# Kernel optimization log

Hardware: AMD Instinct MI355X
Metric: run time of the kernel (lower is better)

Reference implementation:

```python
import jax, jax.numpy as jnp
import numpy as np

DIM_HEAD = 32  # from init_kwargs; scale = dim_head**-0.5 per the Triton kernel


def setup_inputs() -> dict:
    key = jax.random.key(0)
    k1, k2 = jax.random.split(key)
    B, N, dim = 16, 8192, 128
    D = 4 * DIM_HEAD  # heads * dim_head
    x = jax.random.normal(k1, (B, N, dim), dtype=jnp.float32)
    # ParameterList of 16 stages, each Parameter is randn(2, dim, D) * 0.02
    qk_weights = jax.random.normal(k2, (16, 2, dim, D), dtype=jnp.float32) * 0.02
    return {"x": x, "qk_weights": qk_weights}


def reference(x, qk_weights):
    """FFT-inspired butterfly attention.

    At stage s (stride = 2**s), positions are grouped into blocks of 2*stride;
    the first `stride` elements of each block are 'a', the next `stride` are
    their butterfly partners 'b' (b = a + stride). Q/K are projected from the
    ORIGINAL x with per-stage weights; v is the running value buffer (init x).
    For each pair, a 2-way softmax over [qa.ka, qa.kb] mixes (va, vb).
    """
    B, N, dim = x.shape
    logN = int(round(np.log2(N)))
    D = qk_weights.shape[-1]
    scale = DIM_HEAD ** -0.5

    v = x
    for s in range(logN):
        stride = 1 << s
        Wq = qk_weights[s, 0]  # (dim, D)
        Wk = qk_weights[s, 1]
        q = jnp.einsum('bnd,de->bne', x, Wq) * scale  # (B,N,D)
        k = jnp.einsum('bnd,de->bne', x, Wk)
        G = N // (2 * stride)
        qr = q.reshape(B, G, 2, stride, D)
        kr = k.reshape(B, G, 2, stride, D)
        vr = v.reshape(B, G, 2, stride, dim)
        qa = qr[:, :, 0]
        ka, kb = kr[:, :, 0], kr[:, :, 1]
        va, vb = vr[:, :, 0], vr[:, :, 1]
        s_aa = jnp.sum(qa * ka, axis=-1)  # (B,G,stride)
        s_ab = jnp.sum(qa * kb, axis=-1)
        attn = jax.nn.softmax(jnp.stack([s_aa, s_ab], axis=-1), axis=-1)
        w0 = attn[..., 0:1]
        w1 = attn[..., 1:2]
        out_a = w0 * va + w1 * vb
        out_b = w1 * va + w0 * vb
        v = jnp.stack([out_a, out_b], axis=2).reshape(B, N, dim)
    return v
```

## Files before the change

kernel.cpp:

```cpp
#include <hip/hip_runtime.h>
#include <hip/hip_bf16.h>


typedef __bf16 bf16x8 __attribute__((ext_vector_type(8)));
typedef float  f32x4  __attribute__((ext_vector_type(4)));

#define XSTR 136
#define XB_BYTES  (128 * XSTR * 2)
#define PREP_LDS  (2 * XB_BYTES)
#define LDS_W2    XB_BYTES

#define XW 128
#define LDS_W4    (128 * XW * 2)

#define LDS_MIX   (128 * 128 * 4)

#define WS_DWT_OFF (512 * 1024)
#define DWT4_BYTES (13 * 1024 * 4 * 64 * 4)
#define WS_NEED4   (WS_DWT_OFF + DWT4_BYTES)

__device__ __forceinline__ float ubits(unsigned int u) {
    union { unsigned int u; float f; } v; v.u = u; return v.f;
}
__device__ __forceinline__ unsigned short f2bf(float f) {
    union { float f; unsigned int u; } v; v.f = f;
    unsigned int u = v.u;
    return (unsigned short)((u + 0x7fffu + ((u >> 16) & 1u)) >> 16);
}
__device__ __forceinline__ int swzr(int r) { return ((r >> 1) ^ (r >> 2)) & 15; }

#define DPP_MOV_F(x, ctrl) \
    __int_as_float(__builtin_amdgcn_update_dpp(0, __float_as_int(x), (ctrl), 0xF, 0xF, true))

__device__ __forceinline__ float xlane_u(float x, int u, int lane) {
    if (u == 0) return DPP_MOV_F(x, 0xB1);
    if (u == 1) return DPP_MOV_F(x, 0x4E);
    if (u == 2) return __int_as_float(__builtin_amdgcn_ds_swizzle(__float_as_int(x), 0x101F));
    if (u == 3) return __int_as_float(__builtin_amdgcn_ds_swizzle(__float_as_int(x), 0x201F));
    if (u == 4) return __int_as_float(__builtin_amdgcn_ds_swizzle(__float_as_int(x), 0x401F));
    return __int_as_float(__builtin_amdgcn_ds_bpermute((lane ^ 32) << 2, __float_as_int(x)));
}

__global__ __launch_bounds__(512)
void prep_kernel(const float* __restrict__ qkw, unsigned short* __restrict__ PT) {
    extern __shared__ char smem[];
    unsigned short* wkb = (unsigned short*)smem;
    unsigned short* wqb = (unsigned short*)(smem + XB_BYTES);
    const int s = blockIdx.x;
    const float* Wq = qkw + (size_t)s * 32768;
    const float* Wk = Wq + 16384;
    const int tid = threadIdx.x;
    const int rl = tid >> 5, c4 = tid & 31;
#pragma unroll
    for (int j = 0; j < 8; ++j) {
        int r = j * 16 + rl;
        float4 vq = ((const float4*)Wq)[r * 32 + c4];
        float4 vk = ((const float4*)Wk)[r * 32 + c4];
        ushort4 uq; uq.x = f2bf(vq.x); uq.y = f2bf(vq.y); uq.z = f2bf(vq.z); uq.w = f2bf(vq.w);
        ushort4 uk; uk.x = f2bf(vk.x); uk.y = f2bf(vk.y); uk.z = f2bf(vk.z); uk.w = f2bf(vk.w);
        *(ushort4*)(wqb + r * XSTR + c4 * 4) = uq;
        *(ushort4*)(wkb + r * XSTR + c4 * 4) = uk;
    }
    __syncthreads();
    const int lane = tid & 63, w = tid >> 6;
    const int lane15 = lane & 15, quad = lane >> 4;
    f32x4 acc[8] = {};
#pragma unroll
    for (int kk = 0; kk < 4; ++kk) {
        bf16x8 a = *(const bf16x8*)(wkb + (w * 16 + lane15) * XSTR + kk * 32 + quad * 8);
#pragma unroll
        for (int ct = 0; ct < 8; ++ct) {
            bf16x8 b = *(const bf16x8*)(wqb + (ct * 16 + lane15) * XSTR + kk * 32 + quad * 8);
            acc[ct] = __builtin_amdgcn_mfma_f32_16x16x32_bf16(a, b, acc[ct], 0, 0, 0);
        }
    }
    unsigned short* dst = PT + s * 16384;
#pragma unroll
    for (int ct = 0; ct < 8; ++ct) {
        const int kkf = ct >> 1;
        const int qf  = (ct & 1) * 2 + (lane15 >> 3);
        const int e   = lane15 & 7;
#pragma unroll
        for (int r = 0; r < 4; ++r) {
            int fi = (w * 4 + kkf) * 64 + qf * 16 + quad * 4 + r;
            dst[fi * 8 + e] = f2bf(acc[ct][r] * 0.17677669529663687f);
        }
    }
}

__device__ __forceinline__ void stage_xb(unsigned short* xb, const float* xsrc,
                                         int tid, int base, int h_off, int rstride) {
    const int rl = tid >> 5, c4 = tid & 31;
#pragma unroll
    for (int j = 0; j < 8; ++j) {
        int i  = j * 16 + rl;
        int gp = base + (i >> 6) * h_off + (i & 63) * rstride;
        float4 val = ((const float4*)xsrc)[gp * 32 + c4];
        ushort4 us; us.x = f2bf(val.x); us.y = f2bf(val.y);
        us.z = f2bf(val.z); us.w = f2bf(val.w);
        *(ushort4*)(xb + i * XSTR + c4 * 4) = us;
    }
}

__device__ __forceinline__ void stage_xb_swz(unsigned short* xb, const float* xsrc,
                                             int tid, int base, int h_off, int rstride) {
    const int rl = tid >> 5, c4 = tid & 31;
#pragma unroll
    for (int j = 0; j < 8; ++j) {
        int i  = j * 16 + rl;
        int gp = base + (i >> 6) * h_off + (i & 63) * rstride;
        float4 val = ((const float4*)xsrc)[gp * 32 + c4];
        ushort4 us; us.x = f2bf(val.x); us.y = f2bf(val.y);
        us.z = f2bf(val.z); us.w = f2bf(val.w);
        int slot = c4 >> 1, half = c4 & 1;
        *(ushort4*)(xb + i * XW + (((slot ^ swzr(i)) << 3) + half * 4)) = us;
    }
}

template<int NS>
__global__ __launch_bounds__(512, 4)
void weights4_kernel(const float* __restrict__ xsrc,
                     const unsigned short* __restrict__ PT,
                     float* __restrict__ dwt,
                     int s0, int base_mul, int h_off, int rstride)
{
    extern __shared__ char smem[];
    unsigned short* xb = (unsigned short*)smem;

    const int tid  = threadIdx.x;
    const int b    = blockIdx.x >> 6;
    const int sub  = blockIdx.x & 63;
    const int base = b * 8192 + sub * base_mul;

    stage_xb_swz(xb, xsrc, tid, base, h_off, rstride);

    const int lane = tid & 63, w = tid >> 6;
    const int lane15 = lane & 15, quad = lane >> 4;
    const int dh = w >> 1;
    const int ph = w & 1;

    __syncthreads();

#pragma unroll
    for (int u = 0; u < NS; ++u) {
        const int t   = 1 << u;
        const int tm1 = t - 1;

        const uint4* Pf = (const uint4*)PT + (size_t)(s0 + u) * 2048;
        uint4 af[2][4];
#pragma unroll
        for (int mt = 0; mt < 2; ++mt)
#pragma unroll
            for (int kk = 0; kk < 4; ++kk)
                af[mt][kk] = Pf[((dh * 2 + mt) * 4 + kk) * 64 + lane];

        f32x4 acc[2][2] = {};
#pragma unroll
        for (int pg = 0; pg < 2; ++pg) {
            const int p  = (ph * 2 + pg) * 16 + lane15;
            const int ar = ((p & ~tm1) << 1) | (p & tm1);
            const int swa = swzr(ar);
            const unsigned short* brow = xb + ar * XW;
#pragma unroll
            for (int kk = 0; kk < 4; ++kk) {
                bf16x8 bfrag = *(const bf16x8*)(brow + (((kk * 4 + quad) ^ swa) << 3));
#pragma unroll
                for (int mt = 0; mt < 2; ++mt) {
                    union { uint4 u; bf16x8 b; } av; av.u = af[mt][kk];
                    acc[mt][pg] = __builtin_amdgcn_mfma_f32_16x16x32_bf16(av.b, bfrag, acc[mt][pg], 0, 0, 0);
                }
            }
        }

        float sm[2];
#pragma unroll
        for (int pg = 0; pg < 2; ++pg) {
            const int p  = (ph * 2 + pg) * 16 + lane15;
            const int ar = ((p & ~tm1) << 1) | (p & tm1);
            const int br = ar + t;
            const int swa = swzr(ar), swb = swzr(br);
            float s = 0.f;
#pragma unroll
            for (int mt = 0; mt < 2; ++mt) {
                const int slot = dh * 4 + mt * 2 + (quad >> 1);
                uint2 ua = *(const uint2*)(xb + ar * XW + (((slot ^ swa) << 3) + (quad & 1) * 4));
                uint2 ub = *(const uint2*)(xb + br * XW + (((slot ^ swb) << 3) + (quad & 1) * 4));
                float a0 = ubits(ua.x << 16), a1 = ubits(ua.x & 0xffff0000u);
                float a2 = ubits(ua.y << 16), a3 = ubits(ua.y & 0xffff0000u);
                float b0 = ubits(ub.x << 16), b1 = ubits(ub.x & 0xffff0000u);
                float b2 = ubits(ub.y << 16), b3 = ubits(ub.y & 0xffff0000u);
                s += acc[mt][pg][0] * (a0 - b0) + acc[mt][pg][1] * (a1 - b1)
                   + acc[mt][pg][2] * (a2 - b2) + acc[mt][pg][3] * (a3 - b3);
            }
            s += xlane_u(s, 4, lane);
            s += xlane_u(s, 5, lane);
            sm[pg] = s;
        }
        float v = (lane & 16) ? sm[1] : sm[0];
        if (lane < 32)
            dwt[(((size_t)(s0 + u) * 1024 + blockIdx.x) * 4 + dh) * 64 + ph * 32 + (lane & 31)] = v;
    }
}

template<int NS>
__global__ __launch_bounds__(512, 4)
void weights2_kernel(const float* __restrict__ xsrc,
                     const unsigned short* __restrict__ PT,
                     float* __restrict__ dwt,
                     int s0, int base_mul, int h_off, int rstride)
{
    extern __shared__ char smem[];
    unsigned short* xb = (unsigned short*)smem;

    const int tid  = threadIdx.x;
    const int b    = blockIdx.x >> 6;
    const int sub  = blockIdx.x & 63;
    const int base = b * 8192 + sub * base_mul;

    stage_xb(xb, xsrc, tid, base, h_off, rstride);

    const int lane = tid & 63, w = tid >> 6;
    const int lane15 = lane & 15, quad = lane >> 4;
    const int nt = w & 3;
    const int mh = w >> 2;
    const int p  = nt * 16 + lane15;

    __syncthreads();

#pragma unroll
    for (int u = 0; u < NS; ++u) {
        const int t   = 1 << u;
        const int tm1 = t - 1;
        const int ar  = ((p & ~tm1) << 1) | (p & tm1);

        float sm = 0.f;
        {
            const uint4* Pf = (const uint4*)PT + (size_t)(s0 + u) * 2048;
            const unsigned short* brow = xb + ar * XSTR + quad * 8;
            f32x4 acc[4] = {};
#pragma unroll
            for (int kk = 0; kk < 4; ++kk) {
                bf16x8 bfrag = *(const bf16x8*)(brow + kk * 32);
#pragma unroll
                for (int mt = 0; mt < 4; ++mt) {
                    union { uint4 u; bf16x8 b; } av;
                    av.u = Pf[((mh * 4 + mt) * 4 + kk) * 64 + lane];
                    acc[mt] = __builtin_amdgcn_mfma_f32_16x16x32_bf16(av.b, bfrag, acc[mt], 0, 0, 0);
                }
            }
            const unsigned short* da = xb + ar * XSTR + mh * 64 + quad * 4;
            const unsigned short* db = da + t * XSTR;
#pragma unroll
            for (int mt = 0; mt < 4; ++mt) {
                uint2 ua = *(const uint2*)(da + mt * 16);
                uint2 ub = *(const uint2*)(db + mt * 16);
                float a0 = ubits(ua.x << 16), a1 = ubits(ua.x & 0xffff0000u);
                float a2 = ubits(ua.y << 16), a3 = ubits(ua.y & 0xffff0000u);
                float b0 = ubits(ub.x << 16), b1 = ubits(ub.x & 0xffff0000u);
                float b2 = ubits(ub.y << 16), b3 = ubits(ub.y & 0xffff0000u);
                sm += acc[mt][0] * (a0 - b0) + acc[mt][1] * (a1 - b1)
                    + acc[mt][2] * (a2 - b2) + acc[mt][3] * (a3 - b3);
            }
        }
        sm += xlane_u(sm, 4, lane);
        sm += xlane_u(sm, 5, lane);
        if (lane < 16)
            dwt[((size_t)(s0 + u) * 1024 + blockIdx.x) * 128 + mh * 64 + nt * 16 + lane] = sm;
    }
}

template<int NS, int NPART>
__global__ __launch_bounds__(512, 4)
void mix_kernel(const float* __restrict__ vsrc,
                float* __restrict__ vdst,
                const float* __restrict__ dwt,
                int s0, int base_mul, int h_off, int rstride)
{
    extern __shared__ char smem[];
    float* vbuf = (float*)smem;

    const int tid  = threadIdx.x;
    const int b    = blockIdx.x >> 6;
    const int sub  = blockIdx.x & 63;
    const int base = b * 8192 + sub * base_mul;
    const int lane = tid & 63, w = tid >> 6;
    const int rl = tid >> 5, c4 = tid & 31;

    float vlo[16], vhi[16];
    {
        int r0 = 2 * lane, r1 = r0 + 1;
        int gp0 = base + (r0 >> 6) * h_off + (r0 & 63) * rstride;
        int gp1 = base + (r1 >> 6) * h_off + (r1 & 63) * rstride;
        const float* p0 = vsrc + (size_t)gp0 * 128 + w * 16;
        const float* p1 = vsrc + (size_t)gp1 * 128 + w * 16;
#pragma unroll
        for (int j = 0; j < 4; ++j) {
            float4 a = ((const float4*)p0)[j];
            float4 c = ((const float4*)p1)[j];
            vlo[4*j] = a.x; vlo[4*j+1] = a.y; vlo[4*j+2] = a.z; vlo[4*j+3] = a.w;
            vhi[4*j] = c.x; vhi[4*j+1] = c.y; vhi[4*j+2] = c.z; vhi[4*j+3] = c.w;
        }
    }

#pragma unroll
    for (int u = 0; u < NS; ++u) {
        const float* dw = dwt + ((size_t)(s0 + u) * 1024 + blockIdx.x) * (NPART * 64);
        float d = 0.f;
#pragma unroll
        for (int k = 0; k < NPART; ++k) d += dw[k * 64 + lane];
        const float w0 = 1.0f / (1.0f + __expf(-d));
        if (u < NS - 1) {
            const bool isE = ((lane >> u) & 1) == 0;
            const float wk = isE ? w0 : 1.0f - w0;
#pragma unroll
            for (int j = 0; j < 16; ++j) {
                float a = vlo[j], c = vhi[j];
                float s    = a + c;
                float keep = c + wk * (a - c);
                float send = s - keep;
                float ex   = xlane_u(send, u, lane);
                vlo[j] = isE ? keep : ex;
                vhi[j] = isE ? ex : keep;
            }
        } else {
            const float w1 = 1.0f - w0;
#pragma unroll
            for (int j = 0; j < 16; ++j) {
                float a = vlo[j], c = vhi[j];
                float oa = w0 * a + w1 * c;
                vlo[j] = oa;
                vhi[j] = a + c - oa;
            }
        }
    }

    {
        const int FU = NS - 1;
        int r0 = ((lane >> FU) << (FU + 1)) | (lane & ((1 << FU) - 1));
        int r1 = r0 + (1 << FU);
#pragma unroll
        for (int j = 0; j < 4; ++j) {
            float4 a; a.x = vlo[4*j]; a.y = vlo[4*j+1]; a.z = vlo[4*j+2]; a.w = vlo[4*j+3];
            float4 c; c.x = vhi[4*j]; c.y = vhi[4*j+1]; c.z = vhi[4*j+2]; c.w = vhi[4*j+3];
            int slot = w * 4 + j;
            *(float4*)(vbuf + r0 * 128 + ((slot ^ (r0 & 31)) << 2)) = a;
            *(float4*)(vbuf + r1 * 128 + ((slot ^ (r1 & 31)) << 2)) = c;
        }
    }
    __syncthreads();

#pragma unroll
    for (int j = 0; j < 8; ++j) {
        int i  = j * 16 + rl;
        int gp = base + (i >> 6) * h_off + (i & 63) * rstride;
        ((float4*)vdst)[gp * 32 + c4] =
            *(const float4*)(vbuf + i * 128 + (((c4 ^ (i & 31)) << 2)));
    }
}

extern "C" void kernel_launch(void* const* d_in, const int* in_sizes, int n_in,
                              void* d_out, int out_size, void* d_ws, size_t ws_size,
                              hipStream_t stream) {
    const float* x   = (const float*)d_in[0];
    const float* qkw = (const float*)d_in[1];
    float* out = (float*)d_out;
    unsigned short* PT = (unsigned short*)d_ws;
    float* dwt = (float*)((char*)d_ws + WS_DWT_OFF);

    (void)hipFuncSetAttribute((const void*)prep_kernel,
                              hipFuncAttributeMaxDynamicSharedMemorySize, PREP_LDS);

    prep_kernel<<<13, 512, PREP_LDS, stream>>>(qkw, PT);

    if (ws_size >= (size_t)WS_NEED4) {
        (void)hipFuncSetAttribute((const void*)weights4_kernel<7>,
                                  hipFuncAttributeMaxDynamicSharedMemorySize, LDS_W4);
        (void)hipFuncSetAttribute((const void*)weights4_kernel<6>,
                                  hipFuncAttributeMaxDynamicSharedMemorySize, LDS_W4);
        (void)hipFuncSetAttribute((const void*)mix_kernel<7,4>,
                                  hipFuncAttributeMaxDynamicSharedMemorySize, LDS_MIX);
        (void)hipFuncSetAttribute((const void*)mix_kernel<6,4>,
                                  hipFuncAttributeMaxDynamicSharedMemorySize, LDS_MIX);

        weights4_kernel<7><<<1024, 512, LDS_W4, stream>>>(
            x, PT, dwt, 0, 128, 64, 1);
        mix_kernel<7,4><<<1024, 512, LDS_MIX, stream>>>(
            x, out, dwt, 0, 128, 64, 1);
        weights4_kernel<6><<<1024, 512, LDS_W4, stream>>>(
            x, PT, dwt, 7, 2, 1, 128);
        mix_kernel<6,4><<<1024, 512, LDS_MIX, stream>>>(
            out, out, dwt, 7, 2, 1, 128);
    } else {
        (void)hipFuncSetAttribute((const void*)weights2_kernel<7>,
                                  hipFuncAttributeMaxDynamicSharedMemorySize, LDS_W2);
        (void)hipFuncSetAttribute((const void*)weights2_kernel<6>,
                                  hipFuncAttributeMaxDynamicSharedMemorySize, LDS_W2);
        (void)hipFuncSetAttribute((const void*)mix_kernel<7,2>,
                                  hipFuncAttributeMaxDynamicSharedMemorySize, LDS_MIX);
        (void)hipFuncSetAttribute((const void*)mix_kernel<6,2>,
                                  hipFuncAttributeMaxDynamicSharedMemorySize, LDS_MIX);

        weights2_kernel<7><<<1024, 512, LDS_W2, stream>>>(
            x, PT, dwt, 0, 128, 64, 1);
        mix_kernel<7,2><<<1024, 512, LDS_MIX, stream>>>(
            x, out, dwt, 0, 128, 64, 1);
        weights2_kernel<6><<<1024, 512, LDS_W2, stream>>>(
            x, PT, dwt, 7, 2, 1, 128);
        mix_kernel<6,2><<<1024, 512, LDS_MIX, stream>>>(
            out, out, dwt, 7, 2, 1, 128);
    }
}
```

Baseline: 206.0 us.

## Merge both weight-stage kernels into one launch and prefetch next-stage Q/K fragments

```diff
diff --git a/kernel.cpp b/kernel.cpp
--- a/kernel.cpp
+++ b/kernel.cpp
@@ -118,18 +118,14 @@
 }
 
 template<int NS>
-__global__ __launch_bounds__(512, 4)
-void weights4_kernel(const float* __restrict__ xsrc,
-                     const unsigned short* __restrict__ PT,
-                     float* __restrict__ dwt,
-                     int s0, int base_mul, int h_off, int rstride)
+__device__ __forceinline__ void weights_body(const float* __restrict__ xsrc,
+                                             const unsigned short* __restrict__ PT,
+                                             float* __restrict__ dwt,
+                                             unsigned short* xb, int tid, int bid,
+                                             int s0, int base_mul, int h_off, int rstride)
 {
-    extern __shared__ char smem[];
-    unsigned short* xb = (unsigned short*)smem;
-
-    const int tid  = threadIdx.x;
-    const int b    = blockIdx.x >> 6;
-    const int sub  = blockIdx.x & 63;
+    const int b    = bid >> 6;
+    const int sub  = bid & 63;
     const int base = b * 8192 + sub * base_mul;
 
     stage_xb_swz(xb, xsrc, tid, base, h_off, rstride);
@@ -139,20 +135,31 @@
     const int dh = w >> 1;
     const int ph = w & 1;
 
+    uint4 af[2][2][4];
+    {
+        const uint4* Pf = (const uint4*)PT + (size_t)s0 * 2048;
+#pragma unroll
+        for (int mt = 0; mt < 2; ++mt)
+#pragma unroll
+            for (int kk = 0; kk < 4; ++kk)
+                af[0][mt][kk] = Pf[((dh * 2 + mt) * 4 + kk) * 64 + lane];
+    }
     __syncthreads();
 
 #pragma unroll
     for (int u = 0; u < NS; ++u) {
+        const int cur = u & 1, nxt = cur ^ 1;
         const int t   = 1 << u;
         const int tm1 = t - 1;
 
-        const uint4* Pf = (const uint4*)PT + (size_t)(s0 + u) * 2048;
-        uint4 af[2][4];
-#pragma unroll
-        for (int mt = 0; mt < 2; ++mt)
-#pragma unroll
-            for (int kk = 0; kk < 4; ++kk)
-                af[mt][kk] = Pf[((dh * 2 + mt) * 4 + kk) * 64 + lane];
+        if (u + 1 < NS) {
+            const uint4* Pf = (const uint4*)PT + (size_t)(s0 + u + 1) * 2048;
+#pragma unroll
+            for (int mt = 0; mt < 2; ++mt)
+#pragma unroll
+                for (int kk = 0; kk < 4; ++kk)
+                    af[nxt][mt][kk] = Pf[((dh * 2 + mt) * 4 + kk) * 64 + lane];
+        }
 
         f32x4 acc[2][2] = {};
 #pragma unroll
@@ -166,7 +173,7 @@
                 bf16x8 bfrag = *(const bf16x8*)(brow + (((kk * 4 + quad) ^ swa) << 3));
 #pragma unroll
                 for (int mt = 0; mt < 2; ++mt) {
-                    union { uint4 u; bf16x8 b; } av; av.u = af[mt][kk];
+                    union { uint4 u; bf16x8 b; } av; av.u = af[cur][mt][kk];
                     acc[mt][pg] = __builtin_amdgcn_mfma_f32_16x16x32_bf16(av.b, bfrag, acc[mt][pg], 0, 0, 0);
                 }
             }
@@ -198,7 +205,24 @@
         }
         float v = (lane & 16) ? sm[1] : sm[0];
         if (lane < 32)
-            dwt[(((size_t)(s0 + u) * 1024 + blockIdx.x) * 4 + dh) * 64 + ph * 32 + (lane & 31)] = v;
+            dwt[(((size_t)(s0 + u) * 1024 + bid) * 4 + dh) * 64 + ph * 32 + (lane & 31)] = v;
+    }
+}
+
+__global__ __launch_bounds__(512, 4)
+void weights_all_kernel(const float* __restrict__ xsrc,
+                        const unsigned short* __restrict__ PT,
+                        float* __restrict__ dwt)
+{
+    extern __shared__ char smem[];
+    unsigned short* xb = (unsigned short*)smem;
+    const int tid = threadIdx.x;
+    if (blockIdx.x < 1024) {
+        weights_body<7>(xsrc, PT, dwt, xb, tid, blockIdx.x,
+                        0, 128, 64, 1);
+    } else {
+        weights_body<6>(xsrc, PT, dwt, xb, tid, blockIdx.x - 1024,
+                        7, 2, 1, 128);
     }
 }
 
@@ -373,21 +397,17 @@
     prep_kernel<<<13, 512, PREP_LDS, stream>>>(qkw, PT);
 
     if (ws_size >= (size_t)WS_NEED4) {
-        (void)hipFuncSetAttribute((const void*)weights4_kernel<7>,
-                                  hipFuncAttributeMaxDynamicSharedMemorySize, LDS_W4);
-        (void)hipFuncSetAttribute((const void*)weights4_kernel<6>,
+        (void)hipFuncSetAttribute((const void*)weights_all_kernel,
                                   hipFuncAttributeMaxDynamicSharedMemorySize, LDS_W4);
         (void)hipFuncSetAttribute((const void*)mix_kernel<7,4>,
                                   hipFuncAttributeMaxDynamicSharedMemorySize, LDS_MIX);
         (void)hipFuncSetAttribute((const void*)mix_kernel<6,4>,
                                   hipFuncAttributeMaxDynamicSharedMemorySize, LDS_MIX);
 
-        weights4_kernel<7><<<1024, 512, LDS_W4, stream>>>(
-            x, PT, dwt, 0, 128, 64, 1);
+        weights_all_kernel<<<2048, 512, LDS_W4, stream>>>(x, PT, dwt);
+
         mix_kernel<7,4><<<1024, 512, LDS_MIX, stream>>>(
             x, out, dwt, 0, 128, 64, 1);
-        weights4_kernel<6><<<1024, 512, LDS_W4, stream>>>(
-            x, PT, dwt, 7, 2, 1, 128);
         mix_kernel<6,4><<<1024, 512, LDS_MIX, stream>>>(
             out, out, dwt, 7, 2, 1, 128);
     } else {
```

Measured after the change: 197.3 us. -4.2%, faster.
